# Optimization experiments

Measured on AMD Instinct MI355X. Metric: run time of the kernel, lower is better.

The kernel has to match this reference:

```python
import jax, jax.numpy as jnp
import numpy as np

B, N, E, H = 2, 2048, 2048, 16
D = E // H  # head_dim = 128


def setup_inputs() -> dict:
    key = jax.random.key(0)
    k1, k2, k3, k4 = jax.random.split(key, 4)
    x = jax.random.normal(k1, (B, N, E), dtype=jnp.float32)
    Wq = jax.random.normal(k2, (E, E), dtype=jnp.float32) * 0.02
    Wkv = jax.random.normal(k3, (2 * E, E), dtype=jnp.float32) * 0.02
    Wout = jax.random.normal(k4, (E, E), dtype=jnp.float32) * 0.02
    return {"x": x, "Wq": Wq, "Wkv": Wkv, "Wout": Wout}


def reference(x, Wq, Wkv, Wout):
    # projections (torch Linear: y = x @ W.T)
    q = x @ Wq.T                      # [b, n, e]
    kv = x @ Wkv.T                    # [b, n, 2e]
    k, v = jnp.split(kv, 2, axis=-1)  # each [b, n, e]

    def split_heads(t):
        return t.reshape(B, N, H, D).transpose(0, 2, 1, 3)  # [b, h, n, d]

    q, k, v = split_heads(q), split_heads(k), split_heads(v)

    scale = D ** -0.5
    sim = jnp.einsum('bhid,bhjd->bhij', q * scale, k)  # [b, h, n, n]

    # causal mask: triu(j - i + 1) masks strictly-future positions
    mask_value = -jnp.finfo(sim.dtype).max
    causal_mask = jnp.triu(jnp.ones((N, N), dtype=bool), k=1)
    sim = jnp.where(causal_mask, mask_value, sim)

    attn = jax.nn.softmax(sim, axis=-1)
    out = jnp.einsum('bhij,bhjd->bhid', attn, v)  # [b, h, n, d]
    out = out.transpose(0, 2, 1, 3).reshape(B, N, E)
    return out @ Wout.T
```

## Files before the change

kernel.cpp:

```cpp
#include <hip/hip_runtime.h>


typedef __bf16 bf16;
typedef bf16 bf16x2 __attribute__((ext_vector_type(2)));
typedef bf16 bf16x4 __attribute__((ext_vector_type(4)));
typedef bf16 bf16x8 __attribute__((ext_vector_type(8)));
typedef float f32x4 __attribute__((ext_vector_type(4)));
typedef float f32x16 __attribute__((ext_vector_type(16)));

typedef const __attribute__((address_space(1))) void cg_void;
typedef __attribute__((address_space(3))) void lds_void;

#define MFMA16(a, b, c) __builtin_amdgcn_mfma_f32_16x16x32_bf16((a), (b), (c), 0, 0, 0)
#define MFMA32(a, b, c) __builtin_amdgcn_mfma_f32_32x32x16_bf16((a), (b), (c), 0, 0, 0)

__device__ __forceinline__ void async_load16(const bf16* g, bf16* l) {
  __builtin_amdgcn_global_load_lds((cg_void*)g, (lds_void*)l, 16, 0, 0);
}

__global__ __launch_bounds__(256) void cast_all_kernel(
    const float* __restrict__ x, const float* __restrict__ wq,
    const float* __restrict__ wkv, const float* __restrict__ wout,
    bf16* __restrict__ xb, bf16* __restrict__ wqkvb, bf16* __restrict__ woutb) {
  long i = (long)blockIdx.x * 256 + threadIdx.x;
  const float* src; bf16* dst; long off;
  if (i < 1048576)      { src = x;    dst = xb;            off = i; }
  else if (i < 2621440) { src = wq;   dst = wqkvb;         off = i - 1048576;
                          if (off >= 524288) { src = wkv; dst = wqkvb + 4194304; off -= 524288; } }
  else                  { src = wout; dst = woutb;         off = i - 2621440; }
  float4 f0 = ((const float4*)src)[2 * off];
  float4 f1 = ((const float4*)src)[2 * off + 1];
  bf16x8 o;
  o[0] = (bf16)f0.x; o[1] = (bf16)f0.y; o[2] = (bf16)f0.z; o[3] = (bf16)f0.w;
  o[4] = (bf16)f1.x; o[5] = (bf16)f1.y; o[6] = (bf16)f1.z; o[7] = (bf16)f1.w;
  ((bf16x8*)dst)[off] = o;
}

#define STAGE_A(bufi, h, tt) do {                              \
    const bf16* g_ = Ag + (h) * 262144 + (tt) * 64;            \
    bf16* d_ = ldsA + (bufi) * 16384 + (h) * 8192;             \
    async_load16(g_, d_);                                      \
    async_load16(g_ + 131072, d_ + 4096);                      \
  } while (0)
#define STAGE_B(bufi, h, tt) do {                              \
    const bf16* g_ = Bg + (h) * 262144 + (tt) * 64;            \
    bf16* d_ = ldsB + (bufi) * 16384 + (h) * 8192;             \
    async_load16(g_, d_);                                      \
    async_load16(g_ + 131072, d_ + 4096);                      \
  } while (0)
#define STAGE_BS(bufi, tt) do {                                \
    const bf16* g_ = Bg + (tt) * 64;                           \
    bf16* d_ = ldsB + (bufi) * 8192;                           \
    async_load16(g_, d_);                                      \
    async_load16(g_ + 131072, d_ + 4096);                      \
  } while (0)

__global__ __launch_bounds__(512, 2)
void gemm_qk_8phase(const bf16* __restrict__ A, const bf16* __restrict__ B,
                    bf16* __restrict__ qk) {
  __shared__ __attribute__((aligned(16))) bf16 sm[2][2][256][64];
  const int tid = threadIdx.x;
  const int lane = tid & 63;
  const int wid = tid >> 6;
  const int quad = lane >> 4, l15 = lane & 15;
  const int wr = wid >> 2, wc = wid & 3;

  const int lb = (blockIdx.x & 7) * 32 + (blockIdx.x >> 3);
  const int bm = lb >> 4, bn = lb & 15;
  const int m0 = bm * 256, n0 = bn * 256;

  const int srow = tid >> 3;
  const int kswz8 = ((tid & 7) ^ (srow & 7)) * 8;
  const bf16* Ag = A + (size_t)(m0 + srow) * 2048 + kswz8;
  const bf16* Bg = B + (size_t)(n0 + srow) * 2048 + kswz8;
  bf16* ldsA = &sm[0][0][0][0] + tid * 8;
  bf16* ldsB = &sm[1][0][0][0] + tid * 8;

  f32x4 acc[8][4];
#pragma unroll
  for (int i = 0; i < 8; ++i)
#pragma unroll
    for (int j = 0; j < 4; ++j) acc[i][j] = {0.f, 0.f, 0.f, 0.f};

  const int r7 = l15 & 7;
  const int c0 = (quad ^ r7) * 8;
  const int c1 = ((4 + quad) ^ r7) * 8;
  const int arow = (wr * 128 + l15) * 64;
  const int brow = (wc * 64 + l15) * 64;

  STAGE_A(0, 0, 0); STAGE_A(0, 1, 0); STAGE_B(0, 0, 0); STAGE_B(0, 1, 0);
  STAGE_A(1, 0, 1); STAGE_A(1, 1, 1);
  asm volatile("s_waitcnt vmcnt(4)" ::: "memory");
  __builtin_amdgcn_s_barrier();

  for (int t = 0; t < 32; ++t) {
    const int cur = t & 1;
    const bf16* as = &sm[0][0][0][0] + cur * 16384;
    const bf16* bs = &sm[1][0][0][0] + cur * 16384;
    bf16x8 a0[4][2], a1[4][2], b0[2][2], b1[2][2];

#pragma unroll
    for (int i = 0; i < 4; ++i) {
      a0[i][0] = *(const bf16x8*)(as + arow + i * 1024 + c0);
      a0[i][1] = *(const bf16x8*)(as + arow + i * 1024 + c1);
    }
#pragma unroll
    for (int j = 0; j < 2; ++j) {
      b0[j][0] = *(const bf16x8*)(bs + brow + j * 1024 + c0);
      b0[j][1] = *(const bf16x8*)(bs + brow + j * 1024 + c1);
    }
    if (t < 31) STAGE_B(1 - cur, 0, t + 1);
    asm volatile("s_waitcnt lgkmcnt(8)" ::: "memory");
    __builtin_amdgcn_s_barrier();
    asm volatile("s_waitcnt lgkmcnt(0)" ::: "memory");
    __builtin_amdgcn_s_setprio(1);
#pragma unroll
    for (int ks = 0; ks < 2; ++ks)
#pragma unroll
      for (int i = 0; i < 4; ++i)
#pragma unroll
        for (int j = 0; j < 2; ++j) acc[i][j] = MFMA16(a0[i][ks], b0[j][ks], acc[i][j]);
    __builtin_amdgcn_s_setprio(0);
    __builtin_amdgcn_s_barrier();

#pragma unroll
    for (int j = 0; j < 2; ++j) {
      b1[j][0] = *(const bf16x8*)(bs + brow + (2 + j) * 1024 + c0);
      b1[j][1] = *(const bf16x8*)(bs + brow + (2 + j) * 1024 + c1);
    }
    if (t < 31) STAGE_B(1 - cur, 1, t + 1);
    __builtin_amdgcn_s_barrier();
    asm volatile("s_waitcnt lgkmcnt(0)" ::: "memory");
    __builtin_amdgcn_s_setprio(1);
#pragma unroll
    for (int ks = 0; ks < 2; ++ks)
#pragma unroll
      for (int i = 0; i < 4; ++i)
#pragma unroll
        for (int j = 0; j < 2; ++j) acc[i][2 + j] = MFMA16(a0[i][ks], b1[j][ks], acc[i][2 + j]);
    __builtin_amdgcn_s_setprio(0);
    __builtin_amdgcn_s_barrier();

#pragma unroll
    for (int i = 0; i < 4; ++i) {
      a1[i][0] = *(const bf16x8*)(as + arow + (4 + i) * 1024 + c0);
      a1[i][1] = *(const bf16x8*)(as + arow + (4 + i) * 1024 + c1);
    }
    __builtin_amdgcn_s_barrier();
    asm volatile("s_waitcnt lgkmcnt(0)" ::: "memory");
    __builtin_amdgcn_s_setprio(1);
#pragma unroll
    for (int ks = 0; ks < 2; ++ks)
#pragma unroll
      for (int i = 0; i < 4; ++i)
#pragma unroll
        for (int j = 0; j < 2; ++j) acc[4 + i][j] = MFMA16(a1[i][ks], b0[j][ks], acc[4 + i][j]);
    __builtin_amdgcn_s_setprio(0);
    __builtin_amdgcn_s_barrier();

    __builtin_amdgcn_s_setprio(1);
#pragma unroll
    for (int ks = 0; ks < 2; ++ks)
#pragma unroll
      for (int i = 0; i < 4; ++i)
#pragma unroll
        for (int j = 0; j < 2; ++j) acc[4 + i][2 + j] = MFMA16(a1[i][ks], b1[j][ks], acc[4 + i][2 + j]);
    __builtin_amdgcn_s_setprio(0);
    if (t < 30) {
      STAGE_A(cur, 0, t + 2); STAGE_A(cur, 1, t + 2);
      asm volatile("s_waitcnt vmcnt(4)" ::: "memory");
      __builtin_amdgcn_s_barrier();
    } else if (t == 30) {
      asm volatile("s_waitcnt vmcnt(0)" ::: "memory");
      __builtin_amdgcn_s_barrier();
    }
  }

#pragma unroll
  for (int i = 0; i < 8; ++i)
#pragma unroll
    for (int r = 0; r < 4; ++r) {
      const size_t base = (size_t)(m0 + wr * 128 + i * 16 + quad * 4 + r) * 4096
                        + n0 + wc * 64 + l15;
#pragma unroll
      for (int j = 0; j < 4; ++j) qk[base + j * 16] = (bf16)acc[i][j][r];
    }
}

template <int OUTMODE>
__global__ __launch_bounds__(512, 2)
void gemm_thin(const bf16* __restrict__ A, const bf16* __restrict__ B,
               bf16* __restrict__ vt, float* __restrict__ C) {
  __shared__ __attribute__((aligned(16))) bf16 smA[2][256][64];
  __shared__ __attribute__((aligned(16))) bf16 smB[2][128][64];
  const int tid = threadIdx.x;
  const int lane = tid & 63;
  const int wid = tid >> 6;
  const int quad = lane >> 4, l15 = lane & 15;
  const int wr = wid >> 1, wc = wid & 1;

  const int lb = (blockIdx.x & 7) * 32 + (blockIdx.x >> 3);
  const int bm = lb >> 4, bn = lb & 15;
  const int m0 = bm * 256, n0 = bn * 128;

  const int srow = tid >> 3;
  const int kswz8 = ((tid & 7) ^ (srow & 7)) * 8;
  const bf16* Ag = A + (size_t)(m0 + srow) * 2048 + kswz8;
  const bf16* Bg = B + (size_t)(n0 + srow) * 2048 + kswz8;
  bf16* ldsA = &smA[0][0][0] + tid * 8;
  bf16* ldsB = &smB[0][0][0] + tid * 8;

  f32x4 acc[4][4];
#pragma unroll
  for (int i = 0; i < 4; ++i)
#pragma unroll
    for (int j = 0; j < 4; ++j) acc[i][j] = {0.f, 0.f, 0.f, 0.f};

  const int r7 = l15 & 7;
  const int c0 = (quad ^ r7) * 8;
  const int c1 = ((4 + quad) ^ r7) * 8;
  const int arow = (wr * 64 + l15) * 64;
  const int brow = (wc * 64 + l15) * 64;

  STAGE_A(0, 0, 0); STAGE_A(0, 1, 0); STAGE_BS(0, 0);
  STAGE_A(1, 0, 1); STAGE_A(1, 1, 1); STAGE_BS(1, 1);
  asm volatile("s_waitcnt vmcnt(6)" ::: "memory");
  __builtin_amdgcn_s_barrier();

  const bf16* ae = &smA[0][0][0];
  const bf16* ao = &smA[1][0][0];
  const bf16* be = &smB[0][0][0];
  const bf16* bo = &smB[1][0][0];

  for (int u = 0; u < 16; ++u) {
    const int e = 2 * u;
    const bool st = (u < 15);
    bf16x8 afe[4][2], bfe[4][2], afo[4][2], bfo[4][2];

#pragma unroll
    for (int i = 0; i < 4; ++i) {
      afe[i][0] = *(const bf16x8*)(ae + arow + i * 1024 + c0);
      afe[i][1] = *(const bf16x8*)(ae + arow + i * 1024 + c1);
    }
#pragma unroll
    for (int j = 0; j < 4; ++j)
      bfe[j][0] = *(const bf16x8*)(be + brow + j * 1024 + c0);
    asm volatile("s_waitcnt lgkmcnt(0)" ::: "memory");
    __builtin_amdgcn_s_barrier();
    __builtin_amdgcn_s_setprio(1);
#pragma unroll
    for (int i = 0; i < 4; ++i)
#pragma unroll
      for (int j = 0; j < 4; ++j) acc[i][j] = MFMA16(afe[i][0], bfe[j][0], acc[i][j]);
    __builtin_amdgcn_s_setprio(0);
    __builtin_amdgcn_s_barrier();

#pragma unroll
    for (int j = 0; j < 4; ++j)
      bfe[j][1] = *(const bf16x8*)(be + brow + j * 1024 + c1);
    asm volatile("s_waitcnt lgkmcnt(0)" ::: "memory");
    __builtin_amdgcn_s_barrier();
    if (st) { STAGE_A(0, 0, e + 2); STAGE_A(0, 1, e + 2); }
    __builtin_amdgcn_s_setprio(1);
#pragma unroll
    for (int i = 0; i < 4; ++i)
#pragma unroll
      for (int j = 0; j < 4; ++j) acc[i][j] = MFMA16(afe[i][1], bfe[j][1], acc[i][j]);
    __builtin_amdgcn_s_setprio(0);
    if (st) { asm volatile("s_waitcnt vmcnt(4)" ::: "memory"); }
    else    { asm volatile("s_waitcnt vmcnt(0)" ::: "memory"); }
    __builtin_amdgcn_s_barrier();

#pragma unroll
    for (int i = 0; i < 4; ++i) {
      afo[i][0] = *(const bf16x8*)(ao + arow + i * 1024 + c0);
      afo[i][1] = *(const bf16x8*)(ao + arow + i * 1024 + c1);
    }
#pragma unroll
    for (int j = 0; j < 4; ++j)
      bfo[j][0] = *(const bf16x8*)(bo + brow + j * 1024 + c0);
    asm volatile("s_waitcnt lgkmcnt(0)" ::: "memory");
    __builtin_amdgcn_s_barrier();
    if (st) STAGE_BS(0, e + 2);
    __builtin_amdgcn_s_setprio(1);
#pragma unroll
    for (int i = 0; i < 4; ++i)
#pragma unroll
      for (int j = 0; j < 4; ++j) acc[i][j] = MFMA16(afo[i][0], bfo[j][0], acc[i][j]);
    __builtin_amdgcn_s_setprio(0);
    __builtin_amdgcn_s_barrier();

#pragma unroll
    for (int j = 0; j < 4; ++j)
      bfo[j][1] = *(const bf16x8*)(bo + brow + j * 1024 + c1);
    asm volatile("s_waitcnt lgkmcnt(0)" ::: "memory");
    __builtin_amdgcn_s_barrier();
    if (st) { STAGE_A(1, 0, e + 3); STAGE_A(1, 1, e + 3); }
    __builtin_amdgcn_s_setprio(1);
#pragma unroll
    for (int i = 0; i < 4; ++i)
#pragma unroll
      for (int j = 0; j < 4; ++j) acc[i][j] = MFMA16(afo[i][1], bfo[j][1], acc[i][j]);
    __builtin_amdgcn_s_setprio(0);

    if (st) {
      STAGE_BS(1, e + 3);
      asm volatile("s_waitcnt vmcnt(6)" ::: "memory");
      __builtin_amdgcn_s_barrier();
    }
  }

  if constexpr (OUTMODE == 0) {
    __syncthreads();
    bf16* T = &smA[0][0][0];
#pragma unroll
    for (int i = 0; i < 4; ++i)
#pragma unroll
      for (int r = 0; r < 4; ++r) {
        const int nl = wr * 64 + i * 16 + quad * 4 + r;
#pragma unroll
        for (int j = 0; j < 4; ++j) {
          const int fl = wc * 64 + j * 16 + l15;
          T[fl * 256 + ((((nl >> 3) ^ (fl & 31)) << 3) | (nl & 7))] = (bf16)acc[i][j][r];
        }
      }
    __syncthreads();
    const int f0g = n0, nb0 = m0 & 2047, b = m0 >> 11;
#pragma unroll
    for (int c = 0; c < 8; ++c) {
      const int idx = c * 512 + tid;
      const int fl = idx >> 5, nb = idx & 31;
      bf16x8 o = *(const bf16x8*)(T + fl * 256 + ((nb ^ (fl & 31)) << 3));
      *(bf16x8*)(vt + (size_t)(b * 2048 + f0g + fl) * 2048 + nb0 + nb * 8) = o;
    }
  } else {
#pragma unroll
    for (int i = 0; i < 4; ++i) {
#pragma unroll
      for (int r = 0; r < 4; ++r) {
        const size_t base = (size_t)(m0 + wr * 64 + i * 16 + quad * 4 + r) * 2048
                          + n0 + wc * 64 + l15;
#pragma unroll
        for (int j = 0; j < 4; ++j) C[base + j * 16] = (float)acc[i][j][r];
      }
    }
  }
}

__global__ __launch_bounds__(256, 2)
void attn_kernel(const bf16* __restrict__ qk, const bf16* __restrict__ vt,
                 bf16* __restrict__ yb) {
  constexpr int NSEQ = 2048, E = 2048, QKS = 4096;
  __shared__ __attribute__((aligned(16))) bf16 Ks[2][64 * 128];
  __shared__ __attribute__((aligned(16))) bf16 Vs[2][128 * 64];
  const int tid = threadIdx.x;
  const int wave = tid >> 6, lane = tid & 63;
  const int l31 = lane & 31, half = lane >> 5;
  const int id = blockIdx.x;
  const int slot = (id >> 5) & 15;
  const int bh = (id & 7) | (((id >> 3) & 3) << 3);
  const int b = bh >> 4, h = bh & 15;
  const int qt = (slot < 8) ? slot : 23 - slot;
  const float c1 = 0.08838834764831845f * 1.44269504088896f;

  const int krow_s = tid >> 4, kch_s = tid & 15;
  const int vrow_s = tid >> 3, vch_s = tid & 7;
  const bf16* kg = qk + (size_t)(b * NSEQ) * QKS + 2048 + h * 128;
  const bf16* vg = vt + (size_t)b * E * NSEQ + (size_t)(h * 128) * NSEQ;

  const int diag = 2 * qt + (wave >> 1);
  const int ktmax = 2 * qt + 1;

  {
    bf16* kdst = Ks[0] + tid * 8;
    bf16* vdst = Vs[0] + tid * 8;
#pragma unroll
    for (int p = 0; p < 4; ++p) {
      int r = p * 16 + krow_s;
      async_load16(kg + (size_t)r * QKS + (kch_s ^ (r & 7)) * 8, kdst + p * 2048);
    }
#pragma unroll
    for (int p = 0; p < 4; ++p) {
      int r = p * 32 + vrow_s;
      async_load16(vg + (size_t)r * NSEQ + (vch_s ^ (r & 7)) * 8, vdst + p * 2048);
    }
  }

  const int qrow = qt * 128 + wave * 32 + l31;
  bf16x8 qf[8];
  {
    const bf16* qp = qk + (size_t)(b * NSEQ + qrow) * QKS + h * 128 + half * 8;
#pragma unroll
    for (int k8 = 0; k8 < 8; ++k8) qf[k8] = *(const bf16x8*)(qp + k8 * 16);
  }

  float m = -3.0e38f, l = 0.f;
  f32x16 accO[4];
#pragma unroll
  for (int md = 0; md < 4; ++md)
#pragma unroll
    for (int r = 0; r < 16; ++r) accO[md][r] = 0.f;

  union PU { unsigned u; bf16x2 h; };
  union FU { bf16x8 v; unsigned u[4]; };

  const int r31_7 = l31 & 7;

  for (int kt = 0; kt <= ktmax; ++kt) {
    const int cur = kt & 1;
    __syncthreads();

    if (kt < ktmax) {
      const int nxt = kt + 1;
      bf16* kdst = Ks[1 - cur] + tid * 8;
      bf16* vdst = Vs[1 - cur] + tid * 8;
#pragma unroll
      for (int p = 0; p < 4; ++p) {
        int r = p * 16 + krow_s;
        async_load16(kg + (size_t)(nxt * 64 + r) * QKS + (kch_s ^ (r & 7)) * 8, kdst + p * 2048);
      }
#pragma unroll
      for (int p = 0; p < 4; ++p) {
        int r = p * 32 + vrow_s;
        async_load16(vg + (size_t)r * NSEQ + nxt * 64 + (vch_s ^ (r & 7)) * 8, vdst + p * 2048);
      }
    }

    if (kt > diag) continue;

    const bf16* ks = Ks[cur];
    const bf16* vs = Vs[cur];

    bf16x8 kf[2][8];
#pragma unroll
    for (int mt = 0; mt < 2; ++mt) {
      const int row = mt * 32 + l31;
#pragma unroll
      for (int k8 = 0; k8 < 8; ++k8)
        kf[mt][k8] = *(const bf16x8*)(ks + row * 128 + (((k8 * 2 + half) ^ r31_7) * 8));
    }

    f32x16 st[2];
#pragma unroll
    for (int mt = 0; mt < 2; ++mt)
#pragma unroll
      for (int r = 0; r < 16; ++r) st[mt][r] = 0.f;
#pragma unroll
    for (int k8 = 0; k8 < 8; ++k8) {
#pragma unroll
      for (int mt = 0; mt < 2; ++mt)
        st[mt] = MFMA32(kf[mt][k8], qf[k8], st[mt]);
    }

    bf16x8 vf[4][4];
#pragma unroll
    for (int kk = 0; kk < 4; ++kk)
#pragma unroll
      for (int md = 0; md < 4; ++md) {
        const int row = md * 32 + l31;
        vf[kk][md] = *(const bf16x8*)(vs + row * 64 + (((kk * 2 + half) ^ r31_7) * 8));
      }

    if (kt == diag) {
#pragma unroll
      for (int mt = 0; mt < 2; ++mt)
#pragma unroll
        for (int r = 0; r < 16; ++r) {
          int t = kt * 64 + mt * 32 + (r & 3) + 8 * (r >> 2) + 4 * half;
          if (t > qrow) st[mt][r] = -3.0e38f;
        }
    }

    float mx = -3.0e38f;
#pragma unroll
    for (int mt = 0; mt < 2; ++mt)
#pragma unroll
      for (int r = 0; r < 16; ++r) mx = fmaxf(mx, st[mt][r]);
    mx = fmaxf(mx, __shfl_xor(mx, 32));

    const bool noresc = __all((mx - m) * c1 <= 8.0f);
    const float mnew = noresc ? m : fmaxf(m, mx);
    const float mc = mnew * c1;

    float psum = 0.f;
    unsigned pown[2][4][2];
#pragma unroll
    for (int mt = 0; mt < 2; ++mt)
#pragma unroll
      for (int qd = 0; qd < 4; ++qd)
#pragma unroll
        for (int pr = 0; pr < 2; ++pr) {
          float p0 = exp2f(st[mt][qd * 4 + pr * 2] * c1 - mc);
          float p1 = exp2f(st[mt][qd * 4 + pr * 2 + 1] * c1 - mc);
          psum += p0 + p1;
          PU a; a.h[0] = (bf16)p0; a.h[1] = (bf16)p1;
          pown[mt][qd][pr] = a.u;
        }
    psum += __shfl_xor(psum, 32);

    if (!noresc) {
      const float alpha = exp2f((m - mnew) * c1);
      l *= alpha;
      m = mnew;
#pragma unroll
      for (int md = 0; md < 4; ++md)
#pragma unroll
        for (int r = 0; r < 16; ++r) accO[md][r] *= alpha;
    }
    l += psum;

#pragma unroll
    for (int mt = 0; mt < 2; ++mt)
#pragma unroll
      for (int c = 0; c < 2; ++c) {
        const int qa = 2 * c, qb = 2 * c + 1;
        unsigned ra0 = __shfl_xor(pown[mt][qa][0], 32);
        unsigned ra1 = __shfl_xor(pown[mt][qa][1], 32);
        unsigned rb0 = __shfl_xor(pown[mt][qb][0], 32);
        unsigned rb1 = __shfl_xor(pown[mt][qb][1], 32);
        FU f;
        f.u[0] = half ? rb0 : pown[mt][qa][0];
        f.u[1] = half ? rb1 : pown[mt][qa][1];
        f.u[2] = half ? pown[mt][qb][0] : ra0;
        f.u[3] = half ? pown[mt][qb][1] : ra1;
        const int kk = mt * 2 + c;
#pragma unroll
        for (int md = 0; md < 4; ++md)
          accO[md] = MFMA32(vf[kk][md], f.v, accO[md]);
      }
  }

  float invl = 1.0f / l;
  bf16* yp = yb + (size_t)(b * NSEQ + qrow) * E + h * 128;
#pragma unroll
  for (int md = 0; md < 4; ++md)
#pragma unroll
    for (int rq = 0; rq < 4; ++rq) {
      bf16x4 o;
#pragma unroll
      for (int i = 0; i < 4; ++i) o[i] = (bf16)(accO[md][rq * 4 + i] * invl);
      *(bf16x4*)(yp + md * 32 + rq * 8 + half * 4) = o;
    }
}

extern "C" void kernel_launch(void* const* d_in, const int* in_sizes, int n_in,
                              void* d_out, int out_size, void* d_ws, size_t ws_size,
                              hipStream_t stream) {
  const float* x    = (const float*)d_in[0];
  const float* Wq   = (const float*)d_in[1];
  const float* Wkv  = (const float*)d_in[2];
  const float* Wout = (const float*)d_in[3];
  float* out = (float*)d_out;

  constexpr size_t NX = (size_t)2 * 2048 * 2048;
  constexpr size_t NW = (size_t)2048 * 2048;

  bf16* xb     = (bf16*)d_ws;
  bf16* wqkvb  = xb + NX;
  bf16* woutb  = wqkvb + 3 * NW;
  bf16* qk_b   = woutb + NW;
  bf16* y_b    = qk_b + 2 * NX;
  bf16* vt_b   = y_b + NX;

  cast_all_kernel<<<12288, 256, 0, stream>>>(x, Wq, Wkv, Wout, xb, wqkvb, woutb);

  gemm_qk_8phase<<<256, 512, 0, stream>>>(xb, wqkvb, qk_b);
  gemm_thin<0><<<256, 512, 0, stream>>>(xb, wqkvb + (size_t)4096 * 2048, vt_b, nullptr);
  attn_kernel<<<512, 256, 0, stream>>>(qk_b, vt_b, y_b);
  gemm_thin<1><<<256, 512, 0, stream>>>(y_b, woutb, nullptr, out);
}
```

Measured before the change: 352.2 us.

## Split long causal query tiles across KV ranges with a merge kernel

Causal attention work is now split so that query tiles 8–15 are each processed by two blocks covering halves of the key range. A descriptor table assigns roughly equal key-tile counts to each block, which shortens the longest block and evens out the load. Partial outputs, row maxima and row sums for split tiles are written as fp32 into workspace that reuses the dead input-cast buffers. A new merge kernel then combines the pairs with log-sum-exp rescaling. The cost is an extra launch plus extra scratch write and read traffic, and the initial K/V prefetch now starts at each block's own key offset.

```diff
diff --git a/kernel.cpp b/kernel.cpp
--- a/kernel.cpp
+++ b/kernel.cpp
@@ -347,9 +347,22 @@
   }
 }
 
+#define SD(qt, kb, ke, sg) ((qt) | ((kb) << 4) | ((ke) << 10) | ((sg) << 16))
+__device__ const unsigned seg_desc[24] = {
+  SD(7, 0, 16, 2),  SD(15, 0, 16, 0), SD(15, 16, 32, 1),
+  SD(14, 0, 15, 0), SD(14, 15, 30, 1),
+  SD(6, 0, 14, 2),  SD(13, 0, 14, 0), SD(13, 14, 28, 1),
+  SD(12, 0, 13, 0), SD(12, 13, 26, 1),
+  SD(5, 0, 12, 2),  SD(11, 0, 12, 0), SD(11, 12, 24, 1),
+  SD(10, 0, 11, 0), SD(10, 11, 22, 1),
+  SD(4, 0, 10, 2),  SD(9, 0, 10, 0),  SD(9, 10, 20, 1),
+  SD(8, 0, 9, 0),   SD(8, 9, 18, 1),
+  SD(3, 0, 8, 2),   SD(2, 0, 6, 2),   SD(1, 0, 4, 2),   SD(0, 0, 2, 2)
+};
+
 __global__ __launch_bounds__(256, 2)
 void attn_kernel(const bf16* __restrict__ qk, const bf16* __restrict__ vt,
-                 bf16* __restrict__ yb) {
+                 bf16* __restrict__ yb, float* __restrict__ scratch) {
   constexpr int NSEQ = 2048, E = 2048, QKS = 4096;
   __shared__ __attribute__((aligned(16))) bf16 Ks[2][64 * 128];
   __shared__ __attribute__((aligned(16))) bf16 Vs[2][128 * 64];
@@ -357,10 +370,14 @@
   const int wave = tid >> 6, lane = tid & 63;
   const int l31 = lane & 31, half = lane >> 5;
   const int id = blockIdx.x;
-  const int slot = (id >> 5) & 15;
-  const int bh = (id & 7) | (((id >> 3) & 3) << 3);
+  const int sidx = id >> 5;
+  const int bh = id & 31;
+  const unsigned d = seg_desc[sidx];
+  const int qt = d & 15;
+  const int kbeg = (d >> 4) & 63;
+  const int kend = (d >> 10) & 63;
+  const int sg = (d >> 16) & 3;
   const int b = bh >> 4, h = bh & 15;
-  const int qt = (slot < 8) ? slot : 23 - slot;
   const float c1 = 0.08838834764831845f * 1.44269504088896f;
 
   const int krow_s = tid >> 4, kch_s = tid & 15;
@@ -369,7 +386,6 @@
   const bf16* vg = vt + (size_t)b * E * NSEQ + (size_t)(h * 128) * NSEQ;
 
   const int diag = 2 * qt + (wave >> 1);
-  const int ktmax = 2 * qt + 1;
 
   {
     bf16* kdst = Ks[0] + tid * 8;
@@ -377,12 +393,12 @@
 #pragma unroll
     for (int p = 0; p < 4; ++p) {
       int r = p * 16 + krow_s;
-      async_load16(kg + (size_t)r * QKS + (kch_s ^ (r & 7)) * 8, kdst + p * 2048);
+      async_load16(kg + (size_t)(kbeg * 64 + r) * QKS + (kch_s ^ (r & 7)) * 8, kdst + p * 2048);
     }
 #pragma unroll
     for (int p = 0; p < 4; ++p) {
       int r = p * 32 + vrow_s;
-      async_load16(vg + (size_t)r * NSEQ + (vch_s ^ (r & 7)) * 8, vdst + p * 2048);
+      async_load16(vg + (size_t)r * NSEQ + kbeg * 64 + (vch_s ^ (r & 7)) * 8, vdst + p * 2048);
     }
   }
 
@@ -406,11 +422,11 @@
 
   const int r31_7 = l31 & 7;
 
-  for (int kt = 0; kt <= ktmax; ++kt) {
-    const int cur = kt & 1;
+  for (int kt = kbeg; kt < kend; ++kt) {
+    const int cur = (kt - kbeg) & 1;
     __syncthreads();
 
-    if (kt < ktmax) {
+    if (kt + 1 < kend) {
       const int nxt = kt + 1;
       bf16* kdst = Ks[1 - cur] + tid * 8;
       bf16* vdst = Vs[1 - cur] + tid * 8;
@@ -530,17 +546,67 @@
       }
   }
 
-  float invl = 1.0f / l;
-  bf16* yp = yb + (size_t)(b * NSEQ + qrow) * E + h * 128;
-#pragma unroll
-  for (int md = 0; md < 4; ++md)
-#pragma unroll
-    for (int rq = 0; rq < 4; ++rq) {
-      bf16x4 o;
-#pragma unroll
-      for (int i = 0; i < 4; ++i) o[i] = (bf16)(accO[md][rq * 4 + i] * invl);
-      *(bf16x4*)(yp + md * 32 + rq * 8 + half * 4) = o;
-    }
+  if (sg == 2) {
+    float invl = 1.0f / l;
+    bf16* yp = yb + (size_t)(b * NSEQ + qrow) * E + h * 128;
+#pragma unroll
+    for (int md = 0; md < 4; ++md)
+#pragma unroll
+      for (int rq = 0; rq < 4; ++rq) {
+        bf16x4 o;
+#pragma unroll
+        for (int i = 0; i < 4; ++i) o[i] = (bf16)(accO[md][rq * 4 + i] * invl);
+        *(bf16x4*)(yp + md * 32 + rq * 8 + half * 4) = o;
+      }
+  } else {
+    const int slot = ((bh * 8 + (qt - 8)) * 2 + sg);
+    float* fb = scratch + (size_t)slot * 16640;
+    const int row = wave * 32 + l31;
+    fb[16384 + row] = m;
+    fb[16512 + row] = l;
+#pragma unroll
+    for (int md = 0; md < 4; ++md)
+#pragma unroll
+      for (int rq = 0; rq < 4; ++rq) {
+        f32x4 o;
+#pragma unroll
+        for (int i = 0; i < 4; ++i) o[i] = accO[md][rq * 4 + i];
+        *(f32x4*)(fb + row * 128 + md * 32 + rq * 8 + half * 4) = o;
+      }
+  }
+}
+
+__global__ __launch_bounds__(256)
+void attn_merge_kernel(const float* __restrict__ scratch, bf16* __restrict__ yb) {
+  const int blk = blockIdx.x;
+  const int bh = blk >> 3, qt = (blk & 7) + 8;
+  const int b = bh >> 4, h = bh & 15;
+  const float* s0 = scratch + (size_t)(blk * 2) * 16640;
+  const float* s1 = s0 + 16640;
+  const int t = threadIdx.x;
+  const int row = t >> 1, d0 = (t & 1) * 64;
+  const float c1 = 0.08838834764831845f * 1.44269504088896f;
+
+  const float m0 = s0[16384 + row], l0 = s0[16512 + row];
+  const float m1 = s1[16384 + row], l1 = s1[16512 + row];
+  const float M = fmaxf(m0, m1);
+  float a0 = exp2f((m0 - M) * c1);
+  float a1 = exp2f((m1 - M) * c1);
+  const float inv = 1.0f / (a0 * l0 + a1 * l1);
+  a0 *= inv; a1 *= inv;
+
+  bf16* yp = yb + ((size_t)(b * 2048) + qt * 128 + row) * 2048 + h * 128 + d0;
+#pragma unroll
+  for (int i = 0; i < 16; ++i) {
+    float4 o0 = *(const float4*)(s0 + row * 128 + d0 + i * 4);
+    float4 o1 = *(const float4*)(s1 + row * 128 + d0 + i * 4);
+    bf16x4 o;
+    o[0] = (bf16)(a0 * o0.x + a1 * o1.x);
+    o[1] = (bf16)(a0 * o0.y + a1 * o1.y);
+    o[2] = (bf16)(a0 * o0.z + a1 * o1.z);
+    o[3] = (bf16)(a0 * o0.w + a1 * o1.w);
+    *(bf16x4*)(yp + i * 4) = o;
+  }
 }
 
 extern "C" void kernel_launch(void* const* d_in, const int* in_sizes, int n_in,
@@ -561,11 +627,13 @@
   bf16* qk_b   = woutb + NW;
   bf16* y_b    = qk_b + 2 * NX;
   bf16* vt_b   = y_b + NX;
+  float* attn_scr = (float*)d_ws;
 
   cast_all_kernel<<<12288, 256, 0, stream>>>(x, Wq, Wkv, Wout, xb, wqkvb, woutb);
 
   gemm_qk_8phase<<<256, 512, 0, stream>>>(xb, wqkvb, qk_b);
   gemm_thin<0><<<256, 512, 0, stream>>>(xb, wqkvb + (size_t)4096 * 2048, vt_b, nullptr);
-  attn_kernel<<<512, 256, 0, stream>>>(qk_b, vt_b, y_b);
+  attn_kernel<<<768, 256, 0, stream>>>(qk_b, vt_b, y_b, attn_scr);
+  attn_merge_kernel<<<256, 256, 0, stream>>>(attn_scr, y_b);
   gemm_thin<1><<<256, 512, 0, stream>>>(y_b, woutb, nullptr, out);
 }
```

Measured after the change: 356.9 us. About the same (+1.4%).

## Single-buffer V tile and restage K/V pipeline for three blocks per CU

Applied to the files above, without the earlier changes.

The attention kernel drops the V double buffer, cutting LDS per block, and raises launch bounds to three blocks per CU. V for the current tile is now loaded at the start of each iteration and overlapped with the QK^T MFMAs and softmax. Explicit vmcnt waits and extra barriers order the reuse of the single V buffer. V fragments are read from LDS just before each PV MFMA instead of being held in registers, which lowers register pressure at the cost of more barriers per iteration and less prefetch distance for V.

```diff
diff --git a/kernel.cpp b/kernel.cpp
--- a/kernel.cpp
+++ b/kernel.cpp
@@ -347,12 +347,12 @@
   }
 }
 
-__global__ __launch_bounds__(256, 2)
+__global__ __launch_bounds__(256, 3)
 void attn_kernel(const bf16* __restrict__ qk, const bf16* __restrict__ vt,
                  bf16* __restrict__ yb) {
   constexpr int NSEQ = 2048, E = 2048, QKS = 4096;
   __shared__ __attribute__((aligned(16))) bf16 Ks[2][64 * 128];
-  __shared__ __attribute__((aligned(16))) bf16 Vs[2][128 * 64];
+  __shared__ __attribute__((aligned(16))) bf16 Vs[128 * 64];
   const int tid = threadIdx.x;
   const int wave = tid >> 6, lane = tid & 63;
   const int l31 = lane & 31, half = lane >> 5;
@@ -373,16 +373,10 @@
 
   {
     bf16* kdst = Ks[0] + tid * 8;
-    bf16* vdst = Vs[0] + tid * 8;
 #pragma unroll
     for (int p = 0; p < 4; ++p) {
       int r = p * 16 + krow_s;
       async_load16(kg + (size_t)r * QKS + (kch_s ^ (r & 7)) * 8, kdst + p * 2048);
-    }
-#pragma unroll
-    for (int p = 0; p < 4; ++p) {
-      int r = p * 32 + vrow_s;
-      async_load16(vg + (size_t)r * NSEQ + (vch_s ^ (r & 7)) * 8, vdst + p * 2048);
     }
   }
 
@@ -408,126 +402,129 @@
 
   for (int kt = 0; kt <= ktmax; ++kt) {
     const int cur = kt & 1;
-    __syncthreads();
+
+    {
+      bf16* vdst = Vs + tid * 8;
+#pragma unroll
+      for (int p = 0; p < 4; ++p) {
+        int r = p * 32 + vrow_s;
+        async_load16(vg + (size_t)r * NSEQ + kt * 64 + (vch_s ^ (r & 7)) * 8, vdst + p * 2048);
+      }
+    }
+    asm volatile("s_waitcnt vmcnt(8)" ::: "memory");
+    __builtin_amdgcn_s_barrier();
+
+    const bool active = (kt <= diag);
+
+    f32x16 st[2];
+    if (active) {
+      bf16x8 kf[2][8];
+#pragma unroll
+      for (int mt = 0; mt < 2; ++mt) {
+        const int row = mt * 32 + l31;
+#pragma unroll
+        for (int k8 = 0; k8 < 8; ++k8)
+          kf[mt][k8] = *(const bf16x8*)(Ks[cur] + row * 128 + (((k8 * 2 + half) ^ r31_7) * 8));
+      }
+#pragma unroll
+      for (int mt = 0; mt < 2; ++mt)
+#pragma unroll
+        for (int r = 0; r < 16; ++r) st[mt][r] = 0.f;
+#pragma unroll
+      for (int k8 = 0; k8 < 8; ++k8)
+#pragma unroll
+        for (int mt = 0; mt < 2; ++mt)
+          st[mt] = MFMA32(kf[mt][k8], qf[k8], st[mt]);
+    }
 
     if (kt < ktmax) {
-      const int nxt = kt + 1;
       bf16* kdst = Ks[1 - cur] + tid * 8;
-      bf16* vdst = Vs[1 - cur] + tid * 8;
 #pragma unroll
       for (int p = 0; p < 4; ++p) {
         int r = p * 16 + krow_s;
-        async_load16(kg + (size_t)(nxt * 64 + r) * QKS + (kch_s ^ (r & 7)) * 8, kdst + p * 2048);
-      }
-#pragma unroll
-      for (int p = 0; p < 4; ++p) {
-        int r = p * 32 + vrow_s;
-        async_load16(vg + (size_t)r * NSEQ + nxt * 64 + (vch_s ^ (r & 7)) * 8, vdst + p * 2048);
-      }
-    }
-
-    if (kt > diag) continue;
-
-    const bf16* ks = Ks[cur];
-    const bf16* vs = Vs[cur];
-
-    bf16x8 kf[2][8];
-#pragma unroll
-    for (int mt = 0; mt < 2; ++mt) {
-      const int row = mt * 32 + l31;
-#pragma unroll
-      for (int k8 = 0; k8 < 8; ++k8)
-        kf[mt][k8] = *(const bf16x8*)(ks + row * 128 + (((k8 * 2 + half) ^ r31_7) * 8));
-    }
-
-    f32x16 st[2];
-#pragma unroll
-    for (int mt = 0; mt < 2; ++mt)
-#pragma unroll
-      for (int r = 0; r < 16; ++r) st[mt][r] = 0.f;
-#pragma unroll
-    for (int k8 = 0; k8 < 8; ++k8) {
-#pragma unroll
-      for (int mt = 0; mt < 2; ++mt)
-        st[mt] = MFMA32(kf[mt][k8], qf[k8], st[mt]);
-    }
-
-    bf16x8 vf[4][4];
-#pragma unroll
-    for (int kk = 0; kk < 4; ++kk)
-#pragma unroll
-      for (int md = 0; md < 4; ++md) {
-        const int row = md * 32 + l31;
-        vf[kk][md] = *(const bf16x8*)(vs + row * 64 + (((kk * 2 + half) ^ r31_7) * 8));
-      }
-
-    if (kt == diag) {
-#pragma unroll
-      for (int mt = 0; mt < 2; ++mt)
-#pragma unroll
-        for (int r = 0; r < 16; ++r) {
-          int t = kt * 64 + mt * 32 + (r & 3) + 8 * (r >> 2) + 4 * half;
-          if (t > qrow) st[mt][r] = -3.0e38f;
-        }
-    }
-
-    float mx = -3.0e38f;
-#pragma unroll
-    for (int mt = 0; mt < 2; ++mt)
-#pragma unroll
-      for (int r = 0; r < 16; ++r) mx = fmaxf(mx, st[mt][r]);
-    mx = fmaxf(mx, __shfl_xor(mx, 32));
-
-    const bool noresc = __all((mx - m) * c1 <= 8.0f);
-    const float mnew = noresc ? m : fmaxf(m, mx);
-    const float mc = mnew * c1;
+        async_load16(kg + (size_t)((kt + 1) * 64 + r) * QKS + (kch_s ^ (r & 7)) * 8, kdst + p * 2048);
+      }
+    }
 
     float psum = 0.f;
     unsigned pown[2][4][2];
-#pragma unroll
-    for (int mt = 0; mt < 2; ++mt)
-#pragma unroll
-      for (int qd = 0; qd < 4; ++qd)
-#pragma unroll
-        for (int pr = 0; pr < 2; ++pr) {
-          float p0 = exp2f(st[mt][qd * 4 + pr * 2] * c1 - mc);
-          float p1 = exp2f(st[mt][qd * 4 + pr * 2 + 1] * c1 - mc);
-          psum += p0 + p1;
-          PU a; a.h[0] = (bf16)p0; a.h[1] = (bf16)p1;
-          pown[mt][qd][pr] = a.u;
+    bool noresc = true;
+    if (active) {
+      if (kt == diag) {
+#pragma unroll
+        for (int mt = 0; mt < 2; ++mt)
+#pragma unroll
+          for (int r = 0; r < 16; ++r) {
+            int t = kt * 64 + mt * 32 + (r & 3) + 8 * (r >> 2) + 4 * half;
+            if (t > qrow) st[mt][r] = -3.0e38f;
+          }
+      }
+      float mx = -3.0e38f;
+#pragma unroll
+      for (int mt = 0; mt < 2; ++mt)
+#pragma unroll
+        for (int r = 0; r < 16; ++r) mx = fmaxf(mx, st[mt][r]);
+      mx = fmaxf(mx, __shfl_xor(mx, 32));
+
+      noresc = __all((mx - m) * c1 <= 8.0f);
+      const float mnew = noresc ? m : fmaxf(m, mx);
+      const float mc = mnew * c1;
+
+#pragma unroll
+      for (int mt = 0; mt < 2; ++mt)
+#pragma unroll
+        for (int qd = 0; qd < 4; ++qd)
+#pragma unroll
+          for (int pr = 0; pr < 2; ++pr) {
+            float p0 = exp2f(st[mt][qd * 4 + pr * 2] * c1 - mc);
+            float p1 = exp2f(st[mt][qd * 4 + pr * 2 + 1] * c1 - mc);
+            psum += p0 + p1;
+            PU a; a.h[0] = (bf16)p0; a.h[1] = (bf16)p1;
+            pown[mt][qd][pr] = a.u;
+          }
+      psum += __shfl_xor(psum, 32);
+
+      if (!noresc) {
+        const float alpha = exp2f((m - mnew) * c1);
+        l *= alpha;
+        m = mnew;
+#pragma unroll
+        for (int md = 0; md < 4; ++md)
+#pragma unroll
+          for (int r = 0; r < 16; ++r) accO[md][r] *= alpha;
+      }
+      l += psum;
+    }
+
+    if (kt < ktmax) { asm volatile("s_waitcnt vmcnt(8)" ::: "memory"); }
+    else            { asm volatile("s_waitcnt vmcnt(0)" ::: "memory"); }
+    __builtin_amdgcn_s_barrier();
+
+    if (active) {
+#pragma unroll
+      for (int mt = 0; mt < 2; ++mt)
+#pragma unroll
+        for (int c = 0; c < 2; ++c) {
+          const int qa = 2 * c, qb = 2 * c + 1;
+          unsigned ra0 = __shfl_xor(pown[mt][qa][0], 32);
+          unsigned ra1 = __shfl_xor(pown[mt][qa][1], 32);
+          unsigned rb0 = __shfl_xor(pown[mt][qb][0], 32);
+          unsigned rb1 = __shfl_xor(pown[mt][qb][1], 32);
+          FU f;
+          f.u[0] = half ? rb0 : pown[mt][qa][0];
+          f.u[1] = half ? rb1 : pown[mt][qa][1];
+          f.u[2] = half ? pown[mt][qb][0] : ra0;
+          f.u[3] = half ? pown[mt][qb][1] : ra1;
+          const int kk = mt * 2 + c;
+#pragma unroll
+          for (int md = 0; md < 4; ++md) {
+            const int row = md * 32 + l31;
+            bf16x8 vf = *(const bf16x8*)(Vs + row * 64 + (((kk * 2 + half) ^ (row & 7)) * 8));
+            accO[md] = MFMA32(vf, f.v, accO[md]);
+          }
         }
-    psum += __shfl_xor(psum, 32);
-
-    if (!noresc) {
-      const float alpha = exp2f((m - mnew) * c1);
-      l *= alpha;
-      m = mnew;
-#pragma unroll
-      for (int md = 0; md < 4; ++md)
-#pragma unroll
-        for (int r = 0; r < 16; ++r) accO[md][r] *= alpha;
-    }
-    l += psum;
-
-#pragma unroll
-    for (int mt = 0; mt < 2; ++mt)
-#pragma unroll
-      for (int c = 0; c < 2; ++c) {
-        const int qa = 2 * c, qb = 2 * c + 1;
-        unsigned ra0 = __shfl_xor(pown[mt][qa][0], 32);
-        unsigned ra1 = __shfl_xor(pown[mt][qa][1], 32);
-        unsigned rb0 = __shfl_xor(pown[mt][qb][0], 32);
-        unsigned rb1 = __shfl_xor(pown[mt][qb][1], 32);
-        FU f;
-        f.u[0] = half ? rb0 : pown[mt][qa][0];
-        f.u[1] = half ? rb1 : pown[mt][qa][1];
-        f.u[2] = half ? pown[mt][qb][0] : ra0;
-        f.u[3] = half ? pown[mt][qb][1] : ra1;
-        const int kk = mt * 2 + c;
-#pragma unroll
-        for (int md = 0; md < 4; ++md)
-          accO[md] = MFMA32(vf[kk][md], f.v, accO[md]);
-      }
+    }
+    __builtin_amdgcn_s_barrier();
   }
 
   float invl = 1.0f / l;
```

Measured after the change: 396.4 us. +12.6%, slower.
